# Optimization experiments

Measured on AMD Instinct MI355X. Metric: run time of the kernel, lower is better.

The kernel has to match this reference:

```python
import jax, jax.numpy as jnp
import numpy as np

DIM = 768
NUM_HEADS = 12
HEAD_DIM = DIM // NUM_HEADS


def setup_inputs() -> dict:
    key = jax.random.key(0)
    ks = jax.random.split(key, 5)
    scale = 1.0 / np.sqrt(DIM)
    x = jax.random.normal(ks[0], (2, 2048, DIM), dtype=jnp.float32)
    W_qkv = jax.random.normal(ks[1], (DIM, 3 * DIM), dtype=jnp.float32) * scale
    b_qkv = jax.random.normal(ks[2], (3 * DIM,), dtype=jnp.float32) * 0.01
    W_proj = jax.random.normal(ks[3], (DIM, DIM), dtype=jnp.float32) * scale
    b_proj = jax.random.normal(ks[4], (DIM,), dtype=jnp.float32) * 0.01
    return {"x": x, "W_qkv": W_qkv, "b_qkv": b_qkv, "W_proj": W_proj, "b_proj": b_proj}


def reference(x, W_qkv, b_qkv, W_proj, b_proj):
    bsz, seqlen, dim = x.shape
    qkv = x @ W_qkv + b_qkv  # [b, s, 3*dim]
    q, k, v = jnp.split(qkv, 3, axis=-1)
    # [b, h, s, d]
    def split_heads(t):
        return t.reshape(bsz, seqlen, NUM_HEADS, HEAD_DIM).transpose(0, 2, 1, 3)
    q, k, v = split_heads(q), split_heads(k), split_heads(v)
    scores = jnp.einsum("bhqd,bhkd->bhqk", q, k) / np.sqrt(HEAD_DIM).astype(np.float32)
    causal = jnp.tril(jnp.ones((seqlen, seqlen), dtype=bool))
    scores = jnp.where(causal, scores, -jnp.inf)
    attn = jax.nn.softmax(scores, axis=-1)
    out = jnp.einsum("bhqk,bhkd->bhqd", attn, v)
    out = out.transpose(0, 2, 1, 3).reshape(bsz, seqlen, dim)
    return out @ W_proj + b_proj
```

## Files before the change

### kernel.cpp

```cpp
#include <hip/hip_runtime.h>

typedef __bf16 bf16;
typedef __bf16 bf16x4 __attribute__((ext_vector_type(4)));
typedef __bf16 bf16x8 __attribute__((ext_vector_type(8)));
typedef float f32x4 __attribute__((ext_vector_type(4)));

#define DIM 768
#define SEQ 2048
#define BATCH 2
#define NH 12
#define HD 64
#define M_TOT (BATCH*SEQ)
#define NQKV (3*DIM)
#define BK 32

__device__ __forceinline__ f32x4 mfma16(bf16x8 a, bf16x8 b, f32x4 c) {
    return __builtin_amdgcn_mfma_f32_16x16x32_bf16(a, b, c, 0, 0, 0);
}

__device__ __forceinline__ void stage128x32(const bf16* g, int gstride, bf16* lds,
                                            int w, int lane) {
#pragma unroll
    for (int i = 0; i < 2; i++) {
        int p = (w*2 + i)*64 + lane;
        int r = p >> 2, c = p & 3;
        int s = c ^ ((r >> 1) & 3);
        __builtin_amdgcn_global_load_lds(
            (const __attribute__((address_space(1))) unsigned int*)(g + (size_t)r*gstride + s*8),
            (__attribute__((address_space(3))) unsigned int*)(lds + p*8),
            16, 0, 0);
    }
}
__device__ __forceinline__ bf16x8 frag128x32(const bf16* lds, int r, int quad) {
    int c = quad ^ ((r >> 1) & 3);
    return *(const bf16x8*)&lds[r*32 + c*8];
}

#define TQK_TILES ((DIM/32)*(NQKV/32))
#define TP_TILES  ((DIM/32)*(DIM/32))
#define CAST_BLOCKS 768
__global__ __launch_bounds__(256) void prep_kernel(
    const float* __restrict__ x, const float* __restrict__ Wqkv,
    const float* __restrict__ Wproj,
    bf16* __restrict__ xb, bf16* __restrict__ Wqt, bf16* __restrict__ Wpt)
{
    const int bid = blockIdx.x;
    if (bid < TQK_TILES + TP_TILES) {
        const float* src; bf16* dst; int NN, KK, t;
        if (bid < TQK_TILES) { src = Wqkv; dst = Wqt; NN = NQKV; KK = DIM; t = bid; }
        else                 { src = Wproj; dst = Wpt; NN = DIM;  KK = DIM; t = bid - TQK_TILES; }
        const int ntn = NN / 32;
        const int tk = t / ntn, tn = t - tk * ntn;
        __shared__ float tile[32][33];
        const int tx = threadIdx.x & 31, ty = threadIdx.x >> 5;
#pragma unroll
        for (int i = 0; i < 4; i++)
            tile[ty + i*8][tx] = src[(size_t)(tk*32 + ty + i*8)*NN + tn*32 + tx];
        __syncthreads();
#pragma unroll
        for (int i = 0; i < 4; i++)
            dst[(size_t)(tn*32 + ty + i*8)*KK + tk*32 + tx] = (bf16)tile[tx][ty + i*8];
    } else {
        const int b2 = bid - (TQK_TILES + TP_TILES);
        const int N4 = M_TOT*DIM/4;
        for (int i = b2*256 + (int)threadIdx.x; i < N4; i += CAST_BLOCKS*256) {
            float4 v = ((const float4*)x)[i];
            bf16x4 o;
            o[0] = (bf16)v.x; o[1] = (bf16)v.y; o[2] = (bf16)v.z; o[3] = (bf16)v.w;
            *(bf16x4*)&xb[(size_t)i*4] = o;
        }
    }
}

__global__ __launch_bounds__(256) void qkv_gemm(
    const bf16* __restrict__ A,
    const bf16* __restrict__ Bt,
    const float* __restrict__ bias,
    bf16* __restrict__ qkv)
{
    __shared__ bf16 As[128*32];
    __shared__ bf16 Bs[128*32];
    const int K = DIM;
    const int tid = threadIdx.x;
    const int row0 = blockIdx.y * 128, col0 = blockIdx.x * 128;
    const int w = tid >> 6, lane = tid & 63, quad = lane >> 4, l16 = lane & 15;
    const int wy = w >> 1, wx = w & 1;

    f32x4 acc[4][4];
#pragma unroll
    for (int mi = 0; mi < 4; mi++)
#pragma unroll
        for (int ni = 0; ni < 4; ni++)
            acc[mi][ni] = (f32x4){0.f,0.f,0.f,0.f};

    for (int k0 = 0; k0 < K; k0 += BK) {
        __syncthreads();
        stage128x32(A  + (size_t)row0*K + k0, K, As, w, lane);
        stage128x32(Bt + (size_t)col0*K + k0, K, Bs, w, lane);
        __syncthreads();
        bf16x8 af[4], bfv[4];
#pragma unroll
        for (int mi = 0; mi < 4; mi++)
            af[mi] = frag128x32(As, wy*64 + mi*16 + l16, quad);
#pragma unroll
        for (int ni = 0; ni < 4; ni++)
            bfv[ni] = frag128x32(Bs, wx*64 + ni*16 + l16, quad);
#pragma unroll
        for (int mi = 0; mi < 4; mi++)
#pragma unroll
            for (int ni = 0; ni < 4; ni++)
                acc[mi][ni] = mfma16(af[mi], bfv[ni], acc[mi][ni]);
    }

    const int which = col0 / DIM;
    if (which < 2) {
#pragma unroll
        for (int mi = 0; mi < 4; mi++)
#pragma unroll
            for (int ni = 0; ni < 4; ni++)
#pragma unroll
                for (int rr = 0; rr < 4; rr++) {
                    int r = row0 + wy*64 + mi*16 + quad*4 + rr;
                    int c = col0 + wx*64 + ni*16 + l16;
                    float v = acc[mi][ni][rr] + bias[c];
                    int cc = c - which*DIM;
                    int h = cc >> 6, d = cc & 63;
                    int bb = r >> 11, sq = r & (SEQ-1);
                    size_t idx = ((((size_t)which*BATCH + bb)*NH + h)*SEQ + sq)*HD + d;
                    qkv[idx] = (bf16)v;
                }
    } else {
        bf16* Vg = qkv + (size_t)2*BATCH*NH*SEQ*HD;
#pragma unroll
        for (int mi = 0; mi < 4; mi++) {
            int r = row0 + wy*64 + mi*16 + quad*4;
            int bb = r >> 11, sq = r & (SEQ-1);
#pragma unroll
            for (int ni = 0; ni < 4; ni++) {
                int c = col0 + wx*64 + ni*16 + l16;
                int cc = c - 2*DIM;
                int h = cc >> 6, d = cc & 63;
                float bv = bias[c];
                bf16x4 tmp;
#pragma unroll
                for (int rr = 0; rr < 4; rr++)
                    tmp[rr] = (bf16)(acc[mi][ni][rr] + bv);
                size_t idx = (((size_t)bb*NH + h)*HD + d)*SEQ + sq;
                *(bf16x4*)&Vg[idx] = tmp;
            }
        }
    }
}

__global__ __launch_bounds__(256) void attn_kernel(
    const bf16* __restrict__ Q,
    const bf16* __restrict__ Kb,
    const bf16* __restrict__ Vb,
    bf16* __restrict__ attnout,
    bf16* __restrict__ Opart,
    float* __restrict__ lpart)
{
    const int chunk = blockIdx.x;
    const int qt = 31 - (int)blockIdx.y;
    const int bh = blockIdx.z;
    const int b = bh / NH, h = bh - b*NH;

    int kt0, kt1;
    if (qt < 8) { if (chunk) return; kt0 = 0; kt1 = qt; }
    else {
        int hh = (qt + 1) >> 1;
        if (chunk == 0) { kt0 = 0; kt1 = hh - 1; }
        else            { kt0 = hh; kt1 = qt; }
    }

    __shared__ bf16 Kt[64*64];
    __shared__ bf16 Vt[64*64];
    __shared__ bf16 Pl[4][16*72];

    const int tid = threadIdx.x, w = tid >> 6, lane = tid & 63;
    const int quad = lane >> 4, l16 = lane & 15;

    const size_t hoff = (size_t)bh*SEQ*HD;
    const bf16* Qh = Q + hoff;
    const bf16* Kh = Kb + hoff;
    const bf16* Vh = Vb + hoff;

    const int qrow0 = qt*64 + w*16;
    bf16x8 qf0 = *(const bf16x8*)&Qh[(size_t)(qrow0 + l16)*HD + quad*8];
    bf16x8 qf1 = *(const bf16x8*)&Qh[(size_t)(qrow0 + l16)*HD + 32 + quad*8];

    f32x4 of[4];
#pragma unroll
    for (int i = 0; i < 4; i++) of[i] = (f32x4){0.f,0.f,0.f,0.f};
    float lsum = 0.f;

    const int p0 = w*128 + lane;
    const int r0 = p0 >> 3, s0 = (p0 & 7) ^ (r0 & 7);
    const int p1 = p0 + 64;
    const int r1 = p1 >> 3, s1 = (p1 & 7) ^ (r1 & 7);

    uint4 kpre0 = *(const uint4*)&Kh[(size_t)(kt0*64 + r0)*HD + s0*8];
    uint4 kpre1 = *(const uint4*)&Kh[(size_t)(kt0*64 + r1)*HD + s1*8];
    uint4 vpre0 = *(const uint4*)&Vh[(size_t)r0*SEQ + kt0*64 + s0*8];
    uint4 vpre1 = *(const uint4*)&Vh[(size_t)r1*SEQ + kt0*64 + s1*8];

    const float SCL = 0.125f * 1.44269504088896f;
    bf16* pl = &Pl[w][0];

    for (int kt = kt0; kt <= kt1; kt++) {
        __syncthreads();
        *(uint4*)&Kt[p0*8] = kpre0;
        *(uint4*)&Kt[p1*8] = kpre1;
        *(uint4*)&Vt[p0*8] = vpre0;
        *(uint4*)&Vt[p1*8] = vpre1;
        __syncthreads();

        if (kt < kt1) {
            kpre0 = *(const uint4*)&Kh[(size_t)((kt+1)*64 + r0)*HD + s0*8];
            kpre1 = *(const uint4*)&Kh[(size_t)((kt+1)*64 + r1)*HD + s1*8];
            vpre0 = *(const uint4*)&Vh[(size_t)r0*SEQ + (kt+1)*64 + s0*8];
            vpre1 = *(const uint4*)&Vh[(size_t)r1*SEQ + (kt+1)*64 + s1*8];
        }

        f32x4 sf[4];
#pragma unroll
        for (int nt = 0; nt < 4; nt++) sf[nt] = (f32x4){0.f,0.f,0.f,0.f};
#pragma unroll
        for (int nt = 0; nt < 4; nt++) {
            int r = nt*16 + l16;
            bf16x8 kfa = *(const bf16x8*)&Kt[r*64 + ((quad ^ (r&7))*8)];
            bf16x8 kfb = *(const bf16x8*)&Kt[r*64 + (((4+quad) ^ (r&7))*8)];
            sf[nt] = mfma16(kfa, qf0, sf[nt]);
            sf[nt] = mfma16(kfb, qf1, sf[nt]);
        }

        const bool diag = (kt == qt);
        const int qg = qt*64 + w*16 + l16;
#pragma unroll
        for (int nt = 0; nt < 4; nt++) {
            bf16x4 t4;
#pragma unroll
            for (int rr = 0; rr < 4; rr++) {
                float s = sf[nt][rr] * SCL;
                if (diag && (kt*64 + nt*16 + quad*4 + rr) > qg) s = -1e30f;
                float p = __builtin_amdgcn_exp2f(s);
                lsum += p;
                t4[rr] = (bf16)p;
            }
            *(bf16x4*)&pl[l16*72 + nt*16 + quad*4] = t4;
        }

        bf16x8 pa0 = *(const bf16x8*)&pl[l16*72 + quad*8];
        bf16x8 pa1 = *(const bf16x8*)&pl[l16*72 + 32 + quad*8];
#pragma unroll
        for (int dm = 0; dm < 4; dm++) {
            int r = dm*16 + l16;
            bf16x8 vva = *(const bf16x8*)&Vt[r*64 + ((quad ^ (r&7))*8)];
            bf16x8 vvb = *(const bf16x8*)&Vt[r*64 + (((4+quad) ^ (r&7))*8)];
            of[dm] = mfma16(pa0, vva, of[dm]);
            of[dm] = mfma16(pa1, vvb, of[dm]);
        }
    }

    lsum += __shfl_xor(lsum, 16);
    lsum += __shfl_xor(lsum, 32);

    if (qt < 8) {
        float linv[4];
#pragma unroll
        for (int rr = 0; rr < 4; rr++)
            linv[rr] = 1.0f / __shfl(lsum, quad*4 + rr);
#pragma unroll
        for (int rr = 0; rr < 4; rr++) {
            int g = b*SEQ + qt*64 + w*16 + quad*4 + rr;
#pragma unroll
            for (int dm = 0; dm < 4; dm++)
                attnout[(size_t)g*DIM + h*HD + dm*16 + l16] = (bf16)(of[dm][rr] * linv[rr]);
        }
    } else {
        size_t slot = ((size_t)bh*24 + (qt - 8))*2 + chunk;
        bf16* Os = Opart + slot*4096;
        float* ls = lpart + slot*64;
        if (quad == 0) ls[w*16 + l16] = lsum;
#pragma unroll
        for (int rr = 0; rr < 4; rr++) {
            int row = w*16 + quad*4 + rr;
#pragma unroll
            for (int dm = 0; dm < 4; dm++)
                Os[(size_t)row*64 + dm*16 + l16] = (bf16)of[dm][rr];
        }
    }
}

__global__ __launch_bounds__(256) void merge_kernel(
    const bf16* __restrict__ Opart, const float* __restrict__ lpart,
    bf16* __restrict__ attnout)
{
    const int qi = blockIdx.x;
    const int bh = blockIdx.y;
    const int b = bh / NH, h = bh - b*NH;
    const int t = threadIdx.x;
    const int row = t >> 2, cs = t & 3;

    size_t slot0 = ((size_t)bh*24 + qi)*2;
    const bf16* O0 = Opart + slot0*4096 + (size_t)row*64 + cs*16;
    const bf16* O1 = O0 + 4096;
    float inv = 1.0f / (lpart[slot0*64 + row] + lpart[(slot0+1)*64 + row]);

    bf16x8 a0 = *(const bf16x8*)O0;
    bf16x8 a1 = *(const bf16x8*)(O0 + 8);
    bf16x8 b0 = *(const bf16x8*)O1;
    bf16x8 b1 = *(const bf16x8*)(O1 + 8);
    bf16x8 o0, o1;
#pragma unroll
    for (int j = 0; j < 8; j++) {
        o0[j] = (bf16)(((float)a0[j] + (float)b0[j]) * inv);
        o1[j] = (bf16)(((float)a1[j] + (float)b1[j]) * inv);
    }
    size_t o = ((size_t)b*SEQ + (8 + qi)*64 + row)*DIM + h*HD + cs*16;
    *(bf16x8*)&attnout[o]     = o0;
    *(bf16x8*)&attnout[o + 8] = o1;
}

__global__ __launch_bounds__(256) void proj_gemm(
    const bf16* __restrict__ A,
    const bf16* __restrict__ Bt,
    const float* __restrict__ bias,
    float* __restrict__ out)
{
    __shared__ bf16 As[128*32];
    __shared__ bf16 Bs[128*32];
    const int K = DIM;
    const int tid = threadIdx.x;
    const int row0 = blockIdx.y * 128, col0 = blockIdx.x * 128;
    const int w = tid >> 6, lane = tid & 63, quad = lane >> 4, l16 = lane & 15;
    const int wy = w >> 1, wx = w & 1;

    f32x4 acc[4][4];
#pragma unroll
    for (int mi = 0; mi < 4; mi++)
#pragma unroll
        for (int ni = 0; ni < 4; ni++)
            acc[mi][ni] = (f32x4){0.f,0.f,0.f,0.f};

    for (int k0 = 0; k0 < K; k0 += BK) {
        __syncthreads();
        stage128x32(A  + (size_t)row0*K + k0, K, As, w, lane);
        stage128x32(Bt + (size_t)col0*K + k0, K, Bs, w, lane);
        __syncthreads();
        bf16x8 af[4], bfv[4];
#pragma unroll
        for (int mi = 0; mi < 4; mi++)
            af[mi] = frag128x32(As, wy*64 + mi*16 + l16, quad);
#pragma unroll
        for (int ni = 0; ni < 4; ni++)
            bfv[ni] = frag128x32(Bs, wx*64 + ni*16 + l16, quad);
#pragma unroll
        for (int mi = 0; mi < 4; mi++)
#pragma unroll
            for (int ni = 0; ni < 4; ni++)
                acc[mi][ni] = mfma16(af[mi], bfv[ni], acc[mi][ni]);
    }

#pragma unroll
    for (int mi = 0; mi < 4; mi++)
#pragma unroll
        for (int ni = 0; ni < 4; ni++)
#pragma unroll
            for (int rr = 0; rr < 4; rr++) {
                int r = row0 + wy*64 + mi*16 + quad*4 + rr;
                int c = col0 + wx*64 + ni*16 + l16;
                out[(size_t)r*DIM + c] = acc[mi][ni][rr] + bias[c];
            }
}

extern "C" void kernel_launch(void* const* d_in, const int* in_sizes, int n_in,
                              void* d_out, int out_size, void* d_ws, size_t ws_size,
                              hipStream_t stream) {
    const float* x     = (const float*)d_in[0];
    const float* Wqkv  = (const float*)d_in[1];
    const float* bqkv  = (const float*)d_in[2];
    const float* Wproj = (const float*)d_in[3];
    const float* bproj = (const float*)d_in[4];
    float* out = (float*)d_out;

    bf16* xb   = (bf16*)d_ws;
    bf16* Wqt  = xb  + (size_t)M_TOT*DIM;
    bf16* Wpt  = Wqt + (size_t)NQKV*DIM;
    bf16* qkvb = Wpt + (size_t)DIM*DIM;
    bf16* attn = qkvb + (size_t)3*M_TOT*DIM;

    bf16*  Opart = xb;
    float* lpart = (float*)(xb + (size_t)24*24*2*4096);

    const size_t headsz = (size_t)BATCH*NH*SEQ*HD;

    prep_kernel<<<TQK_TILES + TP_TILES + CAST_BLOCKS, 256, 0, stream>>>(
        x, Wqkv, Wproj, xb, Wqt, Wpt);
    qkv_gemm<<<dim3(NQKV/128, M_TOT/128), 256, 0, stream>>>(xb, Wqt, bqkv, qkvb);
    attn_kernel<<<dim3(2, SEQ/64, BATCH*NH), 256, 0, stream>>>(
        qkvb, qkvb + headsz, qkvb + 2*headsz, attn, Opart, lpart);
    merge_kernel<<<dim3(24, BATCH*NH), 256, 0, stream>>>(Opart, lpart, attn);
    proj_gemm<<<dim3(DIM/128, M_TOT/128), 256, 0, stream>>>(attn, Wpt, bproj, out);
}
```

Baseline: 162.3 us.

## Halve attention block to two waves, each handling 32 query rows

The attention kernel now runs with 128 threads (two wavefronts), and each wave processes two 16-row query groups, so every K and V fragment read from LDS feeds twice as many MFMAs. The causal mask branch is also split out so non-diagonal tiles skip the per-element compare. The aim is to cut LDS traffic per MFMA and raise instruction-level parallelism. In exchange, per-thread register use and global staging work roughly double, and with fewer waves per block, latency hiding may suffer.

```diff
diff --git a/kernel.cpp b/kernel.cpp
--- a/kernel.cpp
+++ b/kernel.cpp
@@ -152,7 +152,7 @@
     }
 }
 
-__global__ __launch_bounds__(256) void attn_kernel(
+__global__ __launch_bounds__(128) void attn_kernel(
     const bf16* __restrict__ Q,
     const bf16* __restrict__ Kb,
     const bf16* __restrict__ Vb,
@@ -175,7 +175,7 @@
 
     __shared__ bf16 Kt[64*64];
     __shared__ bf16 Vt[64*64];
-    __shared__ bf16 Pl[4][16*72];
+    __shared__ bf16 Pl[2][2*16*72];
 
     const int tid = threadIdx.x, w = tid >> 6, lane = tid & 63;
     const int quad = lane >> 4, l16 = lane & 15;
@@ -185,109 +185,155 @@
     const bf16* Kh = Kb + hoff;
     const bf16* Vh = Vb + hoff;
 
-    const int qrow0 = qt*64 + w*16;
-    bf16x8 qf0 = *(const bf16x8*)&Qh[(size_t)(qrow0 + l16)*HD + quad*8];
-    bf16x8 qf1 = *(const bf16x8*)&Qh[(size_t)(qrow0 + l16)*HD + 32 + quad*8];
-
-    f32x4 of[4];
-#pragma unroll
-    for (int i = 0; i < 4; i++) of[i] = (f32x4){0.f,0.f,0.f,0.f};
-    float lsum = 0.f;
-
-    const int p0 = w*128 + lane;
-    const int r0 = p0 >> 3, s0 = (p0 & 7) ^ (r0 & 7);
-    const int p1 = p0 + 64;
-    const int r1 = p1 >> 3, s1 = (p1 & 7) ^ (r1 & 7);
-
-    uint4 kpre0 = *(const uint4*)&Kh[(size_t)(kt0*64 + r0)*HD + s0*8];
-    uint4 kpre1 = *(const uint4*)&Kh[(size_t)(kt0*64 + r1)*HD + s1*8];
-    uint4 vpre0 = *(const uint4*)&Vh[(size_t)r0*SEQ + kt0*64 + s0*8];
-    uint4 vpre1 = *(const uint4*)&Vh[(size_t)r1*SEQ + kt0*64 + s1*8];
+    bf16x8 qf[2][2];
+#pragma unroll
+    for (int qg = 0; qg < 2; qg++) {
+        const bf16* qr = &Qh[(size_t)(qt*64 + w*32 + qg*16 + l16)*HD];
+        qf[qg][0] = *(const bf16x8*)&qr[quad*8];
+        qf[qg][1] = *(const bf16x8*)&qr[32 + quad*8];
+    }
+
+    f32x4 of[2][4];
+#pragma unroll
+    for (int qg = 0; qg < 2; qg++)
+#pragma unroll
+        for (int i = 0; i < 4; i++) of[qg][i] = (f32x4){0.f,0.f,0.f,0.f};
+    float lsum[2] = {0.f, 0.f};
+
+    uint4 kpre[4], vpre[4];
+#pragma unroll
+    for (int i = 0; i < 4; i++) {
+        int p = tid + i*128;
+        int r = p >> 3, s = (p & 7) ^ (r & 7);
+        kpre[i] = *(const uint4*)&Kh[(size_t)(kt0*64 + r)*HD + s*8];
+        vpre[i] = *(const uint4*)&Vh[(size_t)r*SEQ + kt0*64 + s*8];
+    }
 
     const float SCL = 0.125f * 1.44269504088896f;
     bf16* pl = &Pl[w][0];
 
     for (int kt = kt0; kt <= kt1; kt++) {
         __syncthreads();
-        *(uint4*)&Kt[p0*8] = kpre0;
-        *(uint4*)&Kt[p1*8] = kpre1;
-        *(uint4*)&Vt[p0*8] = vpre0;
-        *(uint4*)&Vt[p1*8] = vpre1;
+#pragma unroll
+        for (int i = 0; i < 4; i++) {
+            int p = tid + i*128;
+            *(uint4*)&Kt[p*8] = kpre[i];
+            *(uint4*)&Vt[p*8] = vpre[i];
+        }
         __syncthreads();
 
         if (kt < kt1) {
-            kpre0 = *(const uint4*)&Kh[(size_t)((kt+1)*64 + r0)*HD + s0*8];
-            kpre1 = *(const uint4*)&Kh[(size_t)((kt+1)*64 + r1)*HD + s1*8];
-            vpre0 = *(const uint4*)&Vh[(size_t)r0*SEQ + (kt+1)*64 + s0*8];
-            vpre1 = *(const uint4*)&Vh[(size_t)r1*SEQ + (kt+1)*64 + s1*8];
-        }
-
-        f32x4 sf[4];
-#pragma unroll
-        for (int nt = 0; nt < 4; nt++) sf[nt] = (f32x4){0.f,0.f,0.f,0.f};
+#pragma unroll
+            for (int i = 0; i < 4; i++) {
+                int p = tid + i*128;
+                int r = p >> 3, s = (p & 7) ^ (r & 7);
+                kpre[i] = *(const uint4*)&Kh[(size_t)((kt+1)*64 + r)*HD + s*8];
+                vpre[i] = *(const uint4*)&Vh[(size_t)r*SEQ + (kt+1)*64 + s*8];
+            }
+        }
+
+        f32x4 sf[2][4];
+#pragma unroll
+        for (int qg = 0; qg < 2; qg++)
+#pragma unroll
+            for (int nt = 0; nt < 4; nt++) sf[qg][nt] = (f32x4){0.f,0.f,0.f,0.f};
 #pragma unroll
         for (int nt = 0; nt < 4; nt++) {
             int r = nt*16 + l16;
             bf16x8 kfa = *(const bf16x8*)&Kt[r*64 + ((quad ^ (r&7))*8)];
             bf16x8 kfb = *(const bf16x8*)&Kt[r*64 + (((4+quad) ^ (r&7))*8)];
-            sf[nt] = mfma16(kfa, qf0, sf[nt]);
-            sf[nt] = mfma16(kfb, qf1, sf[nt]);
-        }
-
-        const bool diag = (kt == qt);
-        const int qg = qt*64 + w*16 + l16;
-#pragma unroll
-        for (int nt = 0; nt < 4; nt++) {
-            bf16x4 t4;
-#pragma unroll
-            for (int rr = 0; rr < 4; rr++) {
-                float s = sf[nt][rr] * SCL;
-                if (diag && (kt*64 + nt*16 + quad*4 + rr) > qg) s = -1e30f;
-                float p = __builtin_amdgcn_exp2f(s);
-                lsum += p;
-                t4[rr] = (bf16)p;
-            }
-            *(bf16x4*)&pl[l16*72 + nt*16 + quad*4] = t4;
-        }
-
-        bf16x8 pa0 = *(const bf16x8*)&pl[l16*72 + quad*8];
-        bf16x8 pa1 = *(const bf16x8*)&pl[l16*72 + 32 + quad*8];
+#pragma unroll
+            for (int qg = 0; qg < 2; qg++) {
+                sf[qg][nt] = mfma16(kfa, qf[qg][0], sf[qg][nt]);
+                sf[qg][nt] = mfma16(kfb, qf[qg][1], sf[qg][nt]);
+            }
+        }
+
+        if (kt == qt) {
+#pragma unroll
+            for (int qg = 0; qg < 2; qg++) {
+                bf16* pq = pl + qg*1152;
+                const int qrow = qt*64 + w*32 + qg*16 + l16;
+#pragma unroll
+                for (int nt = 0; nt < 4; nt++) {
+                    bf16x4 t4;
+#pragma unroll
+                    for (int rr = 0; rr < 4; rr++) {
+                        float s = sf[qg][nt][rr] * SCL;
+                        if ((kt*64 + nt*16 + quad*4 + rr) > qrow) s = -1e30f;
+                        float p = __builtin_amdgcn_exp2f(s);
+                        lsum[qg] += p;
+                        t4[rr] = (bf16)p;
+                    }
+                    *(bf16x4*)&pq[l16*72 + nt*16 + quad*4] = t4;
+                }
+            }
+        } else {
+#pragma unroll
+            for (int qg = 0; qg < 2; qg++) {
+                bf16* pq = pl + qg*1152;
+#pragma unroll
+                for (int nt = 0; nt < 4; nt++) {
+                    bf16x4 t4;
+#pragma unroll
+                    for (int rr = 0; rr < 4; rr++) {
+                        float p = __builtin_amdgcn_exp2f(sf[qg][nt][rr] * SCL);
+                        lsum[qg] += p;
+                        t4[rr] = (bf16)p;
+                    }
+                    *(bf16x4*)&pq[l16*72 + nt*16 + quad*4] = t4;
+                }
+            }
+        }
+
+        bf16x8 pa[2][2];
+#pragma unroll
+        for (int qg = 0; qg < 2; qg++) {
+            pa[qg][0] = *(const bf16x8*)&pl[qg*1152 + l16*72 + quad*8];
+            pa[qg][1] = *(const bf16x8*)&pl[qg*1152 + l16*72 + 32 + quad*8];
+        }
 #pragma unroll
         for (int dm = 0; dm < 4; dm++) {
             int r = dm*16 + l16;
             bf16x8 vva = *(const bf16x8*)&Vt[r*64 + ((quad ^ (r&7))*8)];
             bf16x8 vvb = *(const bf16x8*)&Vt[r*64 + (((4+quad) ^ (r&7))*8)];
-            of[dm] = mfma16(pa0, vva, of[dm]);
-            of[dm] = mfma16(pa1, vvb, of[dm]);
-        }
-    }
-
-    lsum += __shfl_xor(lsum, 16);
-    lsum += __shfl_xor(lsum, 32);
-
-    if (qt < 8) {
-        float linv[4];
-#pragma unroll
-        for (int rr = 0; rr < 4; rr++)
-            linv[rr] = 1.0f / __shfl(lsum, quad*4 + rr);
-#pragma unroll
-        for (int rr = 0; rr < 4; rr++) {
-            int g = b*SEQ + qt*64 + w*16 + quad*4 + rr;
-#pragma unroll
-            for (int dm = 0; dm < 4; dm++)
-                attnout[(size_t)g*DIM + h*HD + dm*16 + l16] = (bf16)(of[dm][rr] * linv[rr]);
-        }
-    } else {
-        size_t slot = ((size_t)bh*24 + (qt - 8))*2 + chunk;
-        bf16* Os = Opart + slot*4096;
-        float* ls = lpart + slot*64;
-        if (quad == 0) ls[w*16 + l16] = lsum;
-#pragma unroll
-        for (int rr = 0; rr < 4; rr++) {
-            int row = w*16 + quad*4 + rr;
-#pragma unroll
-            for (int dm = 0; dm < 4; dm++)
-                Os[(size_t)row*64 + dm*16 + l16] = (bf16)of[dm][rr];
+#pragma unroll
+            for (int qg = 0; qg < 2; qg++) {
+                of[qg][dm] = mfma16(pa[qg][0], vva, of[qg][dm]);
+                of[qg][dm] = mfma16(pa[qg][1], vvb, of[qg][dm]);
+            }
+        }
+    }
+
+#pragma unroll
+    for (int qg = 0; qg < 2; qg++) {
+        float ls = lsum[qg];
+        ls += __shfl_xor(ls, 16);
+        ls += __shfl_xor(ls, 32);
+        if (qt < 8) {
+            float linv[4];
+#pragma unroll
+            for (int rr = 0; rr < 4; rr++)
+                linv[rr] = 1.0f / __shfl(ls, quad*4 + rr);
+#pragma unroll
+            for (int rr = 0; rr < 4; rr++) {
+                int g = b*SEQ + qt*64 + w*32 + qg*16 + quad*4 + rr;
+#pragma unroll
+                for (int dm = 0; dm < 4; dm++)
+                    attnout[(size_t)g*DIM + h*HD + dm*16 + l16] = (bf16)(of[qg][dm][rr] * linv[rr]);
+            }
+        } else {
+            size_t slot = ((size_t)bh*24 + (qt - 8))*2 + chunk;
+            bf16* Os = Opart + slot*4096;
+            float* lsp = lpart + slot*64;
+            if (quad == 0) lsp[w*32 + qg*16 + l16] = ls;
+#pragma unroll
+            for (int rr = 0; rr < 4; rr++) {
+                int row = w*32 + qg*16 + quad*4 + rr;
+#pragma unroll
+                for (int dm = 0; dm < 4; dm++)
+                    Os[(size_t)row*64 + dm*16 + l16] = (bf16)of[qg][dm][rr];
+            }
         }
     }
 }
@@ -398,7 +444,7 @@
     prep_kernel<<<TQK_TILES + TP_TILES + CAST_BLOCKS, 256, 0, stream>>>(
         x, Wqkv, Wproj, xb, Wqt, Wpt);
     qkv_gemm<<<dim3(NQKV/128, M_TOT/128), 256, 0, stream>>>(xb, Wqt, bqkv, qkvb);
-    attn_kernel<<<dim3(2, SEQ/64, BATCH*NH), 256, 0, stream>>>(
+    attn_kernel<<<dim3(2, SEQ/64, BATCH*NH), 128, 0, stream>>>(
         qkvb, qkvb + headsz, qkvb + 2*headsz, attn, Opart, lpart);
     merge_kernel<<<dim3(24, BATCH*NH), 256, 0, stream>>>(Opart, lpart, attn);
     proj_gemm<<<dim3(DIM/128, M_TOT/128), 256, 0, stream>>>(attn, Wpt, bproj, out);
```

Measured after the change: 233.2 us. 1.44x slower.

## Enlarge attention query tile to 128 rows so each K/V tile is reused twice

Applied to the files above, without the earlier changes.

The attention kernel now processes 128 query rows per block, with each wave handling two 16-row groups that share the same K and V tiles in LDS. This halves the K/V global loads and LDS staging per query row and doubles the MFMA work per synchronisation. The split-K chunking, merge kernel and partial-buffer layout are resized to match. It adds a min-blocks hint to launch_bounds. The cost is more registers per thread, and fewer blocks, so there is less parallelism and coarser causal load balance.

```diff
diff --git a/kernel.cpp b/kernel.cpp
--- a/kernel.cpp
+++ b/kernel.cpp
@@ -152,7 +152,7 @@
     }
 }
 
-__global__ __launch_bounds__(256) void attn_kernel(
+__global__ __launch_bounds__(256, 3) void attn_kernel(
     const bf16* __restrict__ Q,
     const bf16* __restrict__ Kb,
     const bf16* __restrict__ Vb,
@@ -161,21 +161,18 @@
     float* __restrict__ lpart)
 {
     const int chunk = blockIdx.x;
-    const int qt = 31 - (int)blockIdx.y;
+    const int qt2 = 15 - (int)blockIdx.y;
     const int bh = blockIdx.z;
     const int b = bh / NH, h = bh - b*NH;
 
     int kt0, kt1;
-    if (qt < 8) { if (chunk) return; kt0 = 0; kt1 = qt; }
-    else {
-        int hh = (qt + 1) >> 1;
-        if (chunk == 0) { kt0 = 0; kt1 = hh - 1; }
-        else            { kt0 = hh; kt1 = qt; }
-    }
+    if (qt2 < 4) { if (chunk) return; kt0 = 0; kt1 = 2*qt2 + 1; }
+    else if (chunk == 0) { kt0 = 0; kt1 = qt2; }
+    else { kt0 = qt2 + 1; kt1 = 2*qt2 + 1; }
 
     __shared__ bf16 Kt[64*64];
     __shared__ bf16 Vt[64*64];
-    __shared__ bf16 Pl[4][16*72];
+    __shared__ bf16 Pl[4][2*16*72];
 
     const int tid = threadIdx.x, w = tid >> 6, lane = tid & 63;
     const int quad = lane >> 4, l16 = lane & 15;
@@ -185,14 +182,20 @@
     const bf16* Kh = Kb + hoff;
     const bf16* Vh = Vb + hoff;
 
-    const int qrow0 = qt*64 + w*16;
-    bf16x8 qf0 = *(const bf16x8*)&Qh[(size_t)(qrow0 + l16)*HD + quad*8];
-    bf16x8 qf1 = *(const bf16x8*)&Qh[(size_t)(qrow0 + l16)*HD + 32 + quad*8];
-
-    f32x4 of[4];
-#pragma unroll
-    for (int i = 0; i < 4; i++) of[i] = (f32x4){0.f,0.f,0.f,0.f};
-    float lsum = 0.f;
+    bf16x8 qf[2][2];
+#pragma unroll
+    for (int qg = 0; qg < 2; qg++) {
+        const bf16* qr = &Qh[(size_t)(qt2*128 + w*32 + qg*16 + l16)*HD];
+        qf[qg][0] = *(const bf16x8*)&qr[quad*8];
+        qf[qg][1] = *(const bf16x8*)&qr[32 + quad*8];
+    }
+
+    f32x4 of[2][4];
+#pragma unroll
+    for (int qg = 0; qg < 2; qg++)
+#pragma unroll
+        for (int i = 0; i < 4; i++) of[qg][i] = (f32x4){0.f,0.f,0.f,0.f};
+    float lsum[2] = {0.f, 0.f};
 
     const int p0 = w*128 + lane;
     const int r0 = p0 >> 3, s0 = (p0 & 7) ^ (r0 & 7);
@@ -222,72 +225,87 @@
             vpre1 = *(const uint4*)&Vh[(size_t)r1*SEQ + (kt+1)*64 + s1*8];
         }
 
-        f32x4 sf[4];
-#pragma unroll
-        for (int nt = 0; nt < 4; nt++) sf[nt] = (f32x4){0.f,0.f,0.f,0.f};
+        f32x4 sf[2][4];
+#pragma unroll
+        for (int qg = 0; qg < 2; qg++)
+#pragma unroll
+            for (int nt = 0; nt < 4; nt++) sf[qg][nt] = (f32x4){0.f,0.f,0.f,0.f};
 #pragma unroll
         for (int nt = 0; nt < 4; nt++) {
             int r = nt*16 + l16;
             bf16x8 kfa = *(const bf16x8*)&Kt[r*64 + ((quad ^ (r&7))*8)];
             bf16x8 kfb = *(const bf16x8*)&Kt[r*64 + (((4+quad) ^ (r&7))*8)];
-            sf[nt] = mfma16(kfa, qf0, sf[nt]);
-            sf[nt] = mfma16(kfb, qf1, sf[nt]);
-        }
-
-        const bool diag = (kt == qt);
-        const int qg = qt*64 + w*16 + l16;
-#pragma unroll
-        for (int nt = 0; nt < 4; nt++) {
-            bf16x4 t4;
-#pragma unroll
-            for (int rr = 0; rr < 4; rr++) {
-                float s = sf[nt][rr] * SCL;
-                if (diag && (kt*64 + nt*16 + quad*4 + rr) > qg) s = -1e30f;
-                float p = __builtin_amdgcn_exp2f(s);
-                lsum += p;
-                t4[rr] = (bf16)p;
+            sf[0][nt] = mfma16(kfa, qf[0][0], sf[0][nt]);
+            sf[0][nt] = mfma16(kfb, qf[0][1], sf[0][nt]);
+            sf[1][nt] = mfma16(kfa, qf[1][0], sf[1][nt]);
+            sf[1][nt] = mfma16(kfb, qf[1][1], sf[1][nt]);
+        }
+
+        const bool dt = (kt >= 2*qt2);
+#pragma unroll
+        for (int qg = 0; qg < 2; qg++) {
+            bf16* pq = pl + qg*1152;
+            const int qrow = qt2*128 + w*32 + qg*16 + l16;
+#pragma unroll
+            for (int nt = 0; nt < 4; nt++) {
+                bf16x4 t4;
+#pragma unroll
+                for (int rr = 0; rr < 4; rr++) {
+                    float s = sf[qg][nt][rr] * SCL;
+                    if (dt && (kt*64 + nt*16 + quad*4 + rr) > qrow) s = -1e30f;
+                    float p = __builtin_amdgcn_exp2f(s);
+                    lsum[qg] += p;
+                    t4[rr] = (bf16)p;
+                }
+                *(bf16x4*)&pq[l16*72 + nt*16 + quad*4] = t4;
             }
-            *(bf16x4*)&pl[l16*72 + nt*16 + quad*4] = t4;
-        }
-
-        bf16x8 pa0 = *(const bf16x8*)&pl[l16*72 + quad*8];
-        bf16x8 pa1 = *(const bf16x8*)&pl[l16*72 + 32 + quad*8];
+        }
+
+        bf16x8 pa00 = *(const bf16x8*)&pl[l16*72 + quad*8];
+        bf16x8 pa01 = *(const bf16x8*)&pl[l16*72 + 32 + quad*8];
+        bf16x8 pa10 = *(const bf16x8*)&pl[1152 + l16*72 + quad*8];
+        bf16x8 pa11 = *(const bf16x8*)&pl[1152 + l16*72 + 32 + quad*8];
 #pragma unroll
         for (int dm = 0; dm < 4; dm++) {
             int r = dm*16 + l16;
             bf16x8 vva = *(const bf16x8*)&Vt[r*64 + ((quad ^ (r&7))*8)];
             bf16x8 vvb = *(const bf16x8*)&Vt[r*64 + (((4+quad) ^ (r&7))*8)];
-            of[dm] = mfma16(pa0, vva, of[dm]);
-            of[dm] = mfma16(pa1, vvb, of[dm]);
-        }
-    }
-
-    lsum += __shfl_xor(lsum, 16);
-    lsum += __shfl_xor(lsum, 32);
-
-    if (qt < 8) {
-        float linv[4];
-#pragma unroll
-        for (int rr = 0; rr < 4; rr++)
-            linv[rr] = 1.0f / __shfl(lsum, quad*4 + rr);
-#pragma unroll
-        for (int rr = 0; rr < 4; rr++) {
-            int g = b*SEQ + qt*64 + w*16 + quad*4 + rr;
-#pragma unroll
-            for (int dm = 0; dm < 4; dm++)
-                attnout[(size_t)g*DIM + h*HD + dm*16 + l16] = (bf16)(of[dm][rr] * linv[rr]);
-        }
-    } else {
-        size_t slot = ((size_t)bh*24 + (qt - 8))*2 + chunk;
-        bf16* Os = Opart + slot*4096;
-        float* ls = lpart + slot*64;
-        if (quad == 0) ls[w*16 + l16] = lsum;
-#pragma unroll
-        for (int rr = 0; rr < 4; rr++) {
-            int row = w*16 + quad*4 + rr;
-#pragma unroll
-            for (int dm = 0; dm < 4; dm++)
-                Os[(size_t)row*64 + dm*16 + l16] = (bf16)of[dm][rr];
+            of[0][dm] = mfma16(pa00, vva, of[0][dm]);
+            of[0][dm] = mfma16(pa01, vvb, of[0][dm]);
+            of[1][dm] = mfma16(pa10, vva, of[1][dm]);
+            of[1][dm] = mfma16(pa11, vvb, of[1][dm]);
+        }
+    }
+
+#pragma unroll
+    for (int qg = 0; qg < 2; qg++) {
+        float ls = lsum[qg];
+        ls += __shfl_xor(ls, 16);
+        ls += __shfl_xor(ls, 32);
+        if (qt2 < 4) {
+            float linv[4];
+#pragma unroll
+            for (int rr = 0; rr < 4; rr++)
+                linv[rr] = 1.0f / __shfl(ls, quad*4 + rr);
+#pragma unroll
+            for (int rr = 0; rr < 4; rr++) {
+                int g = b*SEQ + qt2*128 + w*32 + qg*16 + quad*4 + rr;
+#pragma unroll
+                for (int dm = 0; dm < 4; dm++)
+                    attnout[(size_t)g*DIM + h*HD + dm*16 + l16] = (bf16)(of[qg][dm][rr] * linv[rr]);
+            }
+        } else {
+            size_t slot = ((size_t)bh*12 + (qt2 - 4))*2 + chunk;
+            bf16* Os = Opart + slot*8192;
+            float* lsp = lpart + slot*128;
+            if (quad == 0) lsp[w*32 + qg*16 + l16] = ls;
+#pragma unroll
+            for (int rr = 0; rr < 4; rr++) {
+                int row = w*32 + qg*16 + quad*4 + rr;
+#pragma unroll
+                for (int dm = 0; dm < 4; dm++)
+                    Os[(size_t)row*64 + dm*16 + l16] = (bf16)of[qg][dm][rr];
+            }
         }
     }
 }
@@ -300,26 +318,34 @@
     const int bh = blockIdx.y;
     const int b = bh / NH, h = bh - b*NH;
     const int t = threadIdx.x;
-    const int row = t >> 2, cs = t & 3;
-
-    size_t slot0 = ((size_t)bh*24 + qi)*2;
-    const bf16* O0 = Opart + slot0*4096 + (size_t)row*64 + cs*16;
-    const bf16* O1 = O0 + 4096;
-    float inv = 1.0f / (lpart[slot0*64 + row] + lpart[(slot0+1)*64 + row]);
+    const int row = t >> 1, half = t & 1;
+
+    size_t slot0 = ((size_t)bh*12 + qi)*2;
+    const bf16* O0 = Opart + slot0*8192 + (size_t)row*64 + half*32;
+    const bf16* O1 = O0 + 8192;
+    float inv = 1.0f / (lpart[slot0*128 + row] + lpart[(slot0+1)*128 + row]);
 
     bf16x8 a0 = *(const bf16x8*)O0;
     bf16x8 a1 = *(const bf16x8*)(O0 + 8);
+    bf16x8 a2 = *(const bf16x8*)(O0 + 16);
+    bf16x8 a3 = *(const bf16x8*)(O0 + 24);
     bf16x8 b0 = *(const bf16x8*)O1;
     bf16x8 b1 = *(const bf16x8*)(O1 + 8);
-    bf16x8 o0, o1;
+    bf16x8 b2 = *(const bf16x8*)(O1 + 16);
+    bf16x8 b3 = *(const bf16x8*)(O1 + 24);
+    bf16x8 o0, o1, o2, o3;
 #pragma unroll
     for (int j = 0; j < 8; j++) {
         o0[j] = (bf16)(((float)a0[j] + (float)b0[j]) * inv);
         o1[j] = (bf16)(((float)a1[j] + (float)b1[j]) * inv);
-    }
-    size_t o = ((size_t)b*SEQ + (8 + qi)*64 + row)*DIM + h*HD + cs*16;
-    *(bf16x8*)&attnout[o]     = o0;
-    *(bf16x8*)&attnout[o + 8] = o1;
+        o2[j] = (bf16)(((float)a2[j] + (float)b2[j]) * inv);
+        o3[j] = (bf16)(((float)a3[j] + (float)b3[j]) * inv);
+    }
+    size_t o = ((size_t)b*SEQ + (4 + qi)*128 + row)*DIM + h*HD + half*32;
+    *(bf16x8*)&attnout[o]      = o0;
+    *(bf16x8*)&attnout[o + 8]  = o1;
+    *(bf16x8*)&attnout[o + 16] = o2;
+    *(bf16x8*)&attnout[o + 24] = o3;
 }
 
 __global__ __launch_bounds__(256) void proj_gemm(
@@ -391,15 +417,15 @@
     bf16* attn = qkvb + (size_t)3*M_TOT*DIM;
 
     bf16*  Opart = xb;
-    float* lpart = (float*)(xb + (size_t)24*24*2*4096);
+    float* lpart = (float*)(xb + (size_t)24*12*2*8192);
 
     const size_t headsz = (size_t)BATCH*NH*SEQ*HD;
 
     prep_kernel<<<TQK_TILES + TP_TILES + CAST_BLOCKS, 256, 0, stream>>>(
         x, Wqkv, Wproj, xb, Wqt, Wpt);
     qkv_gemm<<<dim3(NQKV/128, M_TOT/128), 256, 0, stream>>>(xb, Wqt, bqkv, qkvb);
-    attn_kernel<<<dim3(2, SEQ/64, BATCH*NH), 256, 0, stream>>>(
+    attn_kernel<<<dim3(2, SEQ/128, BATCH*NH), 256, 0, stream>>>(
         qkvb, qkvb + headsz, qkvb + 2*headsz, attn, Opart, lpart);
-    merge_kernel<<<dim3(24, BATCH*NH), 256, 0, stream>>>(Opart, lpart, attn);
+    merge_kernel<<<dim3(12, BATCH*NH), 256, 0, stream>>>(Opart, lpart, attn);
     proj_gemm<<<dim3(DIM/128, M_TOT/128), 256, 0, stream>>>(attn, Wpt, bproj, out);
 }
```

Measured after the change: 164.0 us. About the same (+1.0%).
